# Performance work log

Measured on AMD Instinct MI355X. Metric: run time of the kernel, lower is better.

The kernel has to match this reference:

```python
import jax, jax.numpy as jnp
import numpy as np

EPS = 1e-6  # flax LayerNorm default

def layer_norm(x, scale, bias):
    mean = jnp.mean(x, axis=-1, keepdims=True)
    var = jnp.mean(jnp.square(x - mean), axis=-1, keepdims=True)
    return (x - mean) * jax.lax.rsqrt(var + EPS) * scale + bias

def setup_inputs() -> dict:
    key = jax.random.key(0)
    ks = jax.random.split(key, 8)
    B, M, D, R, H = 8, 8192, 512, 64, 128
    s = 0.02
    return {
        "memory": jax.random.normal(ks[0], (B, M, D), dtype=jnp.float32),
        "output_tokens": jax.random.normal(ks[1], (B, R, D), dtype=jnp.float32),
        # erase path params
        "ln_e_scale": jnp.ones((D,), jnp.float32),
        "ln_e_bias": jnp.zeros((D,), jnp.float32),
        "We1": jax.random.normal(ks[2], (D, H), dtype=jnp.float32) * s,
        "be1": jnp.zeros((H,), jnp.float32),
        "We2": jax.random.normal(ks[3], (H, R), dtype=jnp.float32) * s,
        "be2": jnp.zeros((R,), jnp.float32),
        # add path params
        "ln_a_scale": jnp.ones((D,), jnp.float32),
        "ln_a_bias": jnp.zeros((D,), jnp.float32),
        "Wa1": jax.random.normal(ks[4], (D, H), dtype=jnp.float32) * s,
        "ba1": jnp.zeros((H,), jnp.float32),
        "Wa2": jax.random.normal(ks[5], (H, D), dtype=jnp.float32) * s,
        "ba2": jnp.zeros((D,), jnp.float32),
    }

def reference(memory, output_tokens, ln_e_scale, ln_e_bias, We1, be1, We2, be2,
              ln_a_scale, ln_a_bias, Wa1, ba1, Wa2, ba2):
    # Erase weights: LN -> Dense(H) -> gelu -> Dense(r) -> transpose -> softmax over m
    e = layer_norm(memory, ln_e_scale, ln_e_bias)                  # [b,m,d]
    e = jax.nn.gelu(e @ We1 + be1)                                 # [b,m,H] (tanh approx, flax default)
    e = e @ We2 + be2                                              # [b,m,r]
    erase = jax.nn.softmax(jnp.transpose(e, (0, 2, 1)), axis=-1)   # [b,r,m], softmax over m
    # Add vectors: LN -> Dense(H) -> gelu -> Dense(d)
    a = layer_norm(output_tokens, ln_a_scale, ln_a_bias)           # [b,r,d]
    a = jax.nn.gelu(a @ Wa1 + ba1)                                 # [b,r,H]
    add = a @ Wa2 + ba2                                            # [b,r,d]
    # sum_r erase[b,r,m]*add[b,r,d] -> [b,m,d]; source builds a [b,r,m,d]
    # intermediate; this einsum is the identical math, fused as a batched matmul.
    ea = jnp.einsum('brm,brd->bmd', erase, add)
    # new_memory = memory * (1 - ea) + ea   (erase then add, add_matrix == ea)
    return memory * (1.0 - ea) + ea
```

## Files before the change

### kernel.cpp

```cpp
#include <hip/hip_runtime.h>
#include <hip/hip_bf16.h>
#include <math.h>

#define BB 8
#define MM 8192
#define DD 512
#define RR 64
#define HH 128

typedef __attribute__((ext_vector_type(8))) short bf16x8;
typedef __attribute__((ext_vector_type(4))) short bf16x4;
typedef __attribute__((ext_vector_type(4))) float f32x4;

#define XN_LD 520
#define H_LD  136

__device__ __forceinline__ float gelu_tanh(float x) {
    float u = 0.7978845608028654f * (x + 0.044715f * x * x * x);
    float e = __expf(2.0f * u);
    float t = 1.0f - 2.0f / (e + 1.0f);
    return 0.5f * x * (1.0f + t);
}

__device__ __forceinline__ short f2bf(float f) {
    unsigned int u = __float_as_uint(f);
    unsigned int r = u + 0x7FFFu + ((u >> 16) & 1u);
    return (short)(r >> 16);
}

__global__ __launch_bounds__(256) void prep_weights_kernel(
    const float* __restrict__ We1, const float* __restrict__ We2,
    short* __restrict__ We1T, short* __restrict__ We2T)
{
    int idx = blockIdx.x * 256 + threadIdx.x;
    if (idx < 128 * 512) {
        int n = idx >> 9, k = idx & 511;
        We1T[idx] = f2bf(We1[k * HH + n]);
    } else {
        int j = idx - 128 * 512;
        if (j < 64 * 128) {
            int n = j >> 7, k = j & 127;
            We2T[j] = f2bf(We2[k * RR + n]);
        }
    }
}

__global__ __launch_bounds__(256) void add_path_kernel(
    const float* __restrict__ ot, const float* __restrict__ scale,
    const float* __restrict__ bias, const float* __restrict__ Wa1,
    const float* __restrict__ ba1, const float* __restrict__ Wa2,
    const float* __restrict__ ba2, float* __restrict__ add_out)
{
    int tid = threadIdx.x;
    int b = blockIdx.x >> 6, r = blockIdx.x & 63;
    const float* x = ot + (size_t)(b * RR + r) * DD;
    __shared__ float xs[DD];
    __shared__ float hsm[HH];
    __shared__ float rs[4], rq[4];
    float v0 = x[tid], v1 = x[tid + 256];
    float s = v0 + v1, q = v0 * v0 + v1 * v1;
    #pragma unroll
    for (int off = 32; off > 0; off >>= 1) { s += __shfl_xor(s, off); q += __shfl_xor(q, off); }
    if ((tid & 63) == 0) { rs[tid >> 6] = s; rq[tid >> 6] = q; }
    __syncthreads();
    s = rs[0] + rs[1] + rs[2] + rs[3];
    q = rq[0] + rq[1] + rq[2] + rq[3];
    float mean = s * (1.0f / DD);
    float var = q * (1.0f / DD) - mean * mean;
    float inv = rsqrtf(var + 1e-6f);
    xs[tid]       = (v0 - mean) * inv * scale[tid]       + bias[tid];
    xs[tid + 256] = (v1 - mean) * inv * scale[tid + 256] + bias[tid + 256];
    __syncthreads();
    if (tid < HH) {
        float acc = ba1[tid];
        for (int k = 0; k < DD; k++) acc = fmaf(xs[k], Wa1[k * HH + tid], acc);
        hsm[tid] = gelu_tanh(acc);
    }
    __syncthreads();
    int d0 = tid, d1 = tid + 256;
    float a0 = ba2[d0], a1 = ba2[d1];
    #pragma unroll 4
    for (int k = 0; k < HH; k++) {
        float hk = hsm[k];
        a0 = fmaf(hk, Wa2[k * DD + d0], a0);
        a1 = fmaf(hk, Wa2[k * DD + d1], a1);
    }
    add_out[(size_t)(b * RR + r) * DD + d0] = a0;
    add_out[(size_t)(b * RR + r) * DD + d1] = a1;
}

__global__ __launch_bounds__(256) void erase_mfma_kernel(
    const float* __restrict__ mem, const float* __restrict__ scale,
    const float* __restrict__ bias, const short* __restrict__ We1T,
    const float* __restrict__ be1, const short* __restrict__ We2T,
    const float* __restrict__ be2, float* __restrict__ logits,
    float* __restrict__ pmax, float* __restrict__ psum)
{
    __shared__ short xn[32 * XN_LD];
    short* hsm = xn;

    int tid = threadIdx.x;
    int b = blockIdx.x >> 8;
    int chunk = blockIdx.x & 255;
    int m0 = chunk * 32;

    {
        int row = tid >> 3, sub = tid & 7;
        const float4* srcv = (const float4*)(mem + (size_t)(b * MM + m0 + row) * DD);
        float4 v[16];
        float s = 0.f, q = 0.f;
        #pragma unroll
        for (int j = 0; j < 16; j++) v[j] = srcv[j * 8 + sub];
        #pragma unroll
        for (int j = 0; j < 16; j++) {
            s += v[j].x + v[j].y + v[j].z + v[j].w;
            q += v[j].x*v[j].x + v[j].y*v[j].y + v[j].z*v[j].z + v[j].w*v[j].w;
        }
        #pragma unroll
        for (int off = 1; off <= 4; off <<= 1) { s += __shfl_xor(s, off); q += __shfl_xor(q, off); }
        float mean = s * (1.0f / 512.0f);
        float var = q * (1.0f / 512.0f) - mean * mean;
        float inv = rsqrtf(var + 1e-6f);
        const float4* scv = (const float4*)scale;
        const float4* biv = (const float4*)bias;
        #pragma unroll
        for (int j = 0; j < 16; j++) {
            float4 sc = scv[j * 8 + sub], bi = biv[j * 8 + sub];
            bf16x4 o;
            o[0] = f2bf((v[j].x - mean) * inv * sc.x + bi.x);
            o[1] = f2bf((v[j].y - mean) * inv * sc.y + bi.y);
            o[2] = f2bf((v[j].z - mean) * inv * sc.z + bi.z);
            o[3] = f2bf((v[j].w - mean) * inv * sc.w + bi.w);
            *(bf16x4*)&xn[row * XN_LD + j * 32 + sub * 4] = o;
        }
    }
    __syncthreads();

    int w = tid >> 6, l = tid & 63;
    int lr = l & 15, g = l >> 4, kg = g * 8;

    const short* bp0 = We1T + ((size_t)(w * 32 + lr) << 9) + kg;
    const short* bp1 = bp0 + (16 << 9);
    f32x4 acc00 = {0.f,0.f,0.f,0.f}, acc01 = acc00, acc10 = acc00, acc11 = acc00;
    #pragma unroll 4
    for (int ks = 0; ks < 16; ks++) {
        int k0 = ks * 32;
        bf16x8 a0 = *(const bf16x8*)&xn[lr * XN_LD + k0 + kg];
        bf16x8 a1 = *(const bf16x8*)&xn[(16 + lr) * XN_LD + k0 + kg];
        bf16x8 b0 = *(const bf16x8*)(bp0 + k0);
        bf16x8 b1 = *(const bf16x8*)(bp1 + k0);
        acc00 = __builtin_amdgcn_mfma_f32_16x16x32_bf16(a0, b0, acc00, 0, 0, 0);
        acc10 = __builtin_amdgcn_mfma_f32_16x16x32_bf16(a1, b0, acc10, 0, 0, 0);
        acc01 = __builtin_amdgcn_mfma_f32_16x16x32_bf16(a0, b1, acc01, 0, 0, 0);
        acc11 = __builtin_amdgcn_mfma_f32_16x16x32_bf16(a1, b1, acc11, 0, 0, 0);
    }
    __syncthreads();
    #pragma unroll
    for (int nf = 0; nf < 2; nf++) {
        int col = w * 32 + nf * 16 + lr;
        float bv = be1[col];
        f32x4 A0 = nf ? acc01 : acc00;
        f32x4 A1 = nf ? acc11 : acc10;
        #pragma unroll
        for (int rg = 0; rg < 4; rg++) {
            hsm[(g * 4 + rg) * H_LD + col]        = f2bf(gelu_tanh(A0[rg] + bv));
            hsm[(16 + g * 4 + rg) * H_LD + col]   = f2bf(gelu_tanh(A1[rg] + bv));
        }
    }
    __syncthreads();

    const short* bp2 = We2T + (w * 16 + lr) * 128 + kg;
    f32x4 c0 = {0.f,0.f,0.f,0.f}, c1 = c0;
    #pragma unroll
    for (int ks = 0; ks < 4; ks++) {
        int k0 = ks * 32;
        bf16x8 a0 = *(const bf16x8*)&hsm[lr * H_LD + k0 + kg];
        bf16x8 a1 = *(const bf16x8*)&hsm[(16 + lr) * H_LD + k0 + kg];
        bf16x8 bb = *(const bf16x8*)(bp2 + k0);
        c0 = __builtin_amdgcn_mfma_f32_16x16x32_bf16(a0, bb, c0, 0, 0, 0);
        c1 = __builtin_amdgcn_mfma_f32_16x16x32_bf16(a1, bb, c1, 0, 0, 0);
    }
    {
        int col = w * 16 + lr;
        float bv = be2[col];
        float vv[8];
        #pragma unroll
        for (int rg = 0; rg < 4; rg++) {
            vv[rg]     = c0[rg] + bv;
            vv[4 + rg] = c1[rg] + bv;
            logits[(size_t)(b * MM + m0 + g * 4 + rg) * 64 + col]      = vv[rg];
            logits[(size_t)(b * MM + m0 + 16 + g * 4 + rg) * 64 + col] = vv[4 + rg];
        }
        float mx = vv[0];
        #pragma unroll
        for (int j = 1; j < 8; j++) mx = fmaxf(mx, vv[j]);
        float sm = 0.f;
        #pragma unroll
        for (int j = 0; j < 8; j++) sm += __expf(vv[j] - mx);
        #pragma unroll
        for (int off = 16; off <= 32; off <<= 1) {
            float om = __shfl_xor(mx, off);
            float os = __shfl_xor(sm, off);
            float nm = fmaxf(mx, om);
            sm = sm * __expf(mx - nm) + os * __expf(om - nm);
            mx = nm;
        }
        if (l < 16) {
            pmax[((size_t)b * 256 + chunk) * 64 + col] = mx;
            psum[((size_t)b * 256 + chunk) * 64 + col] = sm;
        }
    }
}

__global__ __launch_bounds__(256) void softmax_finalize_kernel(
    const float* __restrict__ pmax, const float* __restrict__ psum,
    float* __restrict__ rmax, float* __restrict__ rinv)
{
    int b = blockIdx.x;
    int g = threadIdx.x >> 6, r = threadIdx.x & 63;
    float mx = -1e30f, sm = 0.0f;
    for (int ch = g; ch < 256; ch += 4) {
        float m2 = pmax[((size_t)b * 256 + ch) * 64 + r];
        float s2 = psum[((size_t)b * 256 + ch) * 64 + r];
        float nm = fmaxf(mx, m2);
        sm = sm * __expf(mx - nm) + s2 * __expf(m2 - nm);
        mx = nm;
    }
    __shared__ float sx_[4][64], sm_[4][64];
    sx_[g][r] = mx; sm_[g][r] = sm;
    __syncthreads();
    if (threadIdx.x < 64) {
        float M_ = sx_[0][threadIdx.x], S_ = sm_[0][threadIdx.x];
        #pragma unroll
        for (int gg = 1; gg < 4; gg++) {
            float m2 = sx_[gg][threadIdx.x], s2 = sm_[gg][threadIdx.x];
            float nm = fmaxf(M_, m2);
            S_ = S_ * __expf(M_ - nm) + s2 * __expf(m2 - nm);
            M_ = nm;
        }
        rmax[b * 64 + threadIdx.x] = M_;
        rinv[b * 64 + threadIdx.x] = 1.0f / S_;
    }
}

__global__ __launch_bounds__(256) void scale_transpose_kernel(
    const float* __restrict__ add, const float* __restrict__ rinv,
    short* __restrict__ addT)
{
    int b = blockIdx.x >> 3;
    int part = blockIdx.x & 7;
    const float* rv = rinv + b * 64;
    #pragma unroll
    for (int i = 0; i < 16; i++) {
        int idx = part * 4096 + threadIdx.x + i * 256;
        int d = idx >> 6, r = idx & 63;
        addT[(size_t)b * 32768 + idx] =
            f2bf(add[((size_t)b * 64 + r) * 512 + d] * rv[r]);
    }
}

__global__ __launch_bounds__(256, 4) void apply_mfma_kernel(
    const float* __restrict__ mem, const float* __restrict__ logits,
    const short* __restrict__ addT, const float* __restrict__ rmax,
    float* __restrict__ out)
{
    int tid = threadIdx.x;
    int w = tid >> 6, l = tid & 63;
    int b = blockIdx.x >> 7;
    int mt = blockIdx.x & 127;
    int m0 = mt * 64;
    int lr = l & 15, kg = (l >> 4) * 8;
    int nbase = w * 128;
    const short* aT = addT + (size_t)b * 512 * 64;

    float rm0[8], rm1[8];
    #pragma unroll
    for (int j = 0; j < 8; j++) {
        rm0[j] = rmax[b * 64 + kg + j];
        rm1[j] = rmax[b * 64 + 32 + kg + j];
    }

    for (int ms = 0; ms < 4; ms++) {
        float mv[8][4];
        #pragma unroll
        for (int nf = 0; nf < 8; nf++) {
            int d = nbase + nf * 16 + lr;
            #pragma unroll
            for (int rg = 0; rg < 4; rg++) {
                int m = m0 + ms * 16 + (l >> 4) * 4 + rg;
                mv[nf][rg] = mem[(size_t)(b * MM + m) * DD + d];
            }
        }
        int mrow = m0 + ms * 16 + lr;
        const float* lp = logits + (size_t)(b * MM + mrow) * 64 + kg;
        float w0[8], w1[8];
        #pragma unroll
        for (int j = 0; j < 8; j++) {
            w0[j] = __expf(lp[j]      - rm0[j]);
            w1[j] = __expf(lp[32 + j] - rm1[j]);
        }
        bf16x8 a0, a1;
        #pragma unroll
        for (int j = 0; j < 8; j++) { a0[j] = f2bf(w0[j]); a1[j] = f2bf(w1[j]); }

        f32x4 acc[8];
        #pragma unroll
        for (int nf = 0; nf < 8; nf++) {
            int d = nbase + nf * 16 + lr;
            bf16x8 b0 = *(const bf16x8*)&aT[d * 64 + kg];
            bf16x8 b1 = *(const bf16x8*)&aT[d * 64 + 32 + kg];
            f32x4 c = (f32x4){0.f, 0.f, 0.f, 0.f};
            c = __builtin_amdgcn_mfma_f32_16x16x32_bf16(a0, b0, c, 0, 0, 0);
            c = __builtin_amdgcn_mfma_f32_16x16x32_bf16(a1, b1, c, 0, 0, 0);
            acc[nf] = c;
        }
        #pragma unroll
        for (int nf = 0; nf < 8; nf++) {
            int d = nbase + nf * 16 + lr;
            #pragma unroll
            for (int rg = 0; rg < 4; rg++) {
                int m = m0 + ms * 16 + (l >> 4) * 4 + rg;
                size_t off = (size_t)(b * MM + m) * DD + d;
                float mvv = mv[nf][rg];
                out[off] = fmaf(acc[nf][rg], 1.0f - mvv, mvv);
            }
        }
    }
}

extern "C" void kernel_launch(void* const* d_in, const int* in_sizes, int n_in,
                              void* d_out, int out_size, void* d_ws, size_t ws_size,
                              hipStream_t stream) {
    const float* memory = (const float*)d_in[0];
    const float* ot     = (const float*)d_in[1];
    const float* ln_e_s = (const float*)d_in[2];
    const float* ln_e_b = (const float*)d_in[3];
    const float* We1    = (const float*)d_in[4];
    const float* be1    = (const float*)d_in[5];
    const float* We2    = (const float*)d_in[6];
    const float* be2    = (const float*)d_in[7];
    const float* ln_a_s = (const float*)d_in[8];
    const float* ln_a_b = (const float*)d_in[9];
    const float* Wa1    = (const float*)d_in[10];
    const float* ba1    = (const float*)d_in[11];
    const float* Wa2    = (const float*)d_in[12];
    const float* ba2    = (const float*)d_in[13];
    float* out = (float*)d_out;

    float* ws      = (float*)d_ws;
    float* add_ws  = ws;
    float* logits  = ws + 262144;
    float* pmaxw   = ws + 262144 + 4194304;
    float* psumw   = pmaxw + 131072;
    float* rmaxw   = psumw + 131072;
    float* rinvw   = rmaxw + 512;
    short* We1T    = (short*)(rinvw + 512);
    short* We2T    = We1T + 128 * 512;
    short* addT    = We2T + 64 * 128;

    hipLaunchKernelGGL(prep_weights_kernel, dim3(288), dim3(256), 0, stream,
                       We1, We2, We1T, We2T);
    hipLaunchKernelGGL(add_path_kernel, dim3(BB * RR), dim3(256), 0, stream,
                       ot, ln_a_s, ln_a_b, Wa1, ba1, Wa2, ba2, add_ws);
    hipLaunchKernelGGL(erase_mfma_kernel, dim3(BB * 256), dim3(256), 0, stream,
                       memory, ln_e_s, ln_e_b, We1T, be1, We2T, be2, logits, pmaxw, psumw);
    hipLaunchKernelGGL(softmax_finalize_kernel, dim3(BB), dim3(256), 0, stream,
                       pmaxw, psumw, rmaxw, rinvw);
    hipLaunchKernelGGL(scale_transpose_kernel, dim3(BB * 8), dim3(256), 0, stream,
                       add_ws, rinvw, addT);
    hipLaunchKernelGGL(apply_mfma_kernel, dim3(BB * 128), dim3(256), 0, stream,
                       memory, logits, addT, rmaxw, out);
}
```

Before: 195.5 us.

## Double erase-kernel threads and halve apply-kernel tile to raise parallelism

The erase kernel now runs 512 threads per block. Each wave computes one 16-column slice of the first GEMM, and in the second GEMM waves split across the two 16-row halves and the four column groups. Partial softmax stats are now emitted per half-chunk, so the finalize kernel reduces over 512 chunks. The apply kernel now uses 32-row tiles with twice as many blocks, giving more blocks to fill the GPU at the cost of less reuse of addT per block and more partial-stat traffic.

Measured after the change: 198.1 us. Within noise of the previous version (+1.3%).

```diff
diff --git a/kernel.cpp b/kernel.cpp
--- a/kernel.cpp
+++ b/kernel.cpp
@@ -89,7 +89,7 @@
     add_out[(size_t)(b * RR + r) * DD + d1] = a1;
 }
 
-__global__ __launch_bounds__(256) void erase_mfma_kernel(
+__global__ __launch_bounds__(512) void erase_mfma_kernel(
     const float* __restrict__ mem, const float* __restrict__ scale,
     const float* __restrict__ bias, const short* __restrict__ We1T,
     const float* __restrict__ be1, const short* __restrict__ We2T,
@@ -105,33 +105,33 @@
     int m0 = chunk * 32;
 
     {
-        int row = tid >> 3, sub = tid & 7;
+        int row = tid >> 4, sub = tid & 15;
         const float4* srcv = (const float4*)(mem + (size_t)(b * MM + m0 + row) * DD);
-        float4 v[16];
+        float4 v[8];
+        #pragma unroll
+        for (int j = 0; j < 8; j++) v[j] = srcv[j * 16 + sub];
         float s = 0.f, q = 0.f;
         #pragma unroll
-        for (int j = 0; j < 16; j++) v[j] = srcv[j * 8 + sub];
-        #pragma unroll
-        for (int j = 0; j < 16; j++) {
+        for (int j = 0; j < 8; j++) {
             s += v[j].x + v[j].y + v[j].z + v[j].w;
             q += v[j].x*v[j].x + v[j].y*v[j].y + v[j].z*v[j].z + v[j].w*v[j].w;
         }
         #pragma unroll
-        for (int off = 1; off <= 4; off <<= 1) { s += __shfl_xor(s, off); q += __shfl_xor(q, off); }
+        for (int off = 1; off <= 8; off <<= 1) { s += __shfl_xor(s, off); q += __shfl_xor(q, off); }
         float mean = s * (1.0f / 512.0f);
         float var = q * (1.0f / 512.0f) - mean * mean;
         float inv = rsqrtf(var + 1e-6f);
         const float4* scv = (const float4*)scale;
         const float4* biv = (const float4*)bias;
         #pragma unroll
-        for (int j = 0; j < 16; j++) {
-            float4 sc = scv[j * 8 + sub], bi = biv[j * 8 + sub];
+        for (int j = 0; j < 8; j++) {
+            float4 sc = scv[j * 16 + sub], bi = biv[j * 16 + sub];
             bf16x4 o;
             o[0] = f2bf((v[j].x - mean) * inv * sc.x + bi.x);
             o[1] = f2bf((v[j].y - mean) * inv * sc.y + bi.y);
             o[2] = f2bf((v[j].z - mean) * inv * sc.z + bi.z);
             o[3] = f2bf((v[j].w - mean) * inv * sc.w + bi.w);
-            *(bf16x4*)&xn[row * XN_LD + j * 32 + sub * 4] = o;
+            *(bf16x4*)&xn[row * XN_LD + (j * 16 + sub) * 4] = o;
         }
     }
     __syncthreads();
@@ -139,64 +139,50 @@
     int w = tid >> 6, l = tid & 63;
     int lr = l & 15, g = l >> 4, kg = g * 8;
 
-    const short* bp0 = We1T + ((size_t)(w * 32 + lr) << 9) + kg;
-    const short* bp1 = bp0 + (16 << 9);
-    f32x4 acc00 = {0.f,0.f,0.f,0.f}, acc01 = acc00, acc10 = acc00, acc11 = acc00;
+    const short* bp0 = We1T + ((size_t)(w * 16 + lr) << 9) + kg;
+    f32x4 acc0 = {0.f,0.f,0.f,0.f}, acc1 = acc0;
     #pragma unroll 4
     for (int ks = 0; ks < 16; ks++) {
         int k0 = ks * 32;
         bf16x8 a0 = *(const bf16x8*)&xn[lr * XN_LD + k0 + kg];
         bf16x8 a1 = *(const bf16x8*)&xn[(16 + lr) * XN_LD + k0 + kg];
         bf16x8 b0 = *(const bf16x8*)(bp0 + k0);
-        bf16x8 b1 = *(const bf16x8*)(bp1 + k0);
-        acc00 = __builtin_amdgcn_mfma_f32_16x16x32_bf16(a0, b0, acc00, 0, 0, 0);
-        acc10 = __builtin_amdgcn_mfma_f32_16x16x32_bf16(a1, b0, acc10, 0, 0, 0);
-        acc01 = __builtin_amdgcn_mfma_f32_16x16x32_bf16(a0, b1, acc01, 0, 0, 0);
-        acc11 = __builtin_amdgcn_mfma_f32_16x16x32_bf16(a1, b1, acc11, 0, 0, 0);
-    }
-    __syncthreads();
-    #pragma unroll
-    for (int nf = 0; nf < 2; nf++) {
-        int col = w * 32 + nf * 16 + lr;
+        acc0 = __builtin_amdgcn_mfma_f32_16x16x32_bf16(a0, b0, acc0, 0, 0, 0);
+        acc1 = __builtin_amdgcn_mfma_f32_16x16x32_bf16(a1, b0, acc1, 0, 0, 0);
+    }
+    __syncthreads();
+    {
+        int col = w * 16 + lr;
         float bv = be1[col];
-        f32x4 A0 = nf ? acc01 : acc00;
-        f32x4 A1 = nf ? acc11 : acc10;
         #pragma unroll
         for (int rg = 0; rg < 4; rg++) {
-            hsm[(g * 4 + rg) * H_LD + col]        = f2bf(gelu_tanh(A0[rg] + bv));
-            hsm[(16 + g * 4 + rg) * H_LD + col]   = f2bf(gelu_tanh(A1[rg] + bv));
-        }
-    }
-    __syncthreads();
-
-    const short* bp2 = We2T + (w * 16 + lr) * 128 + kg;
-    f32x4 c0 = {0.f,0.f,0.f,0.f}, c1 = c0;
+            hsm[(g * 4 + rg) * H_LD + col]      = f2bf(gelu_tanh(acc0[rg] + bv));
+            hsm[(16 + g * 4 + rg) * H_LD + col] = f2bf(gelu_tanh(acc1[rg] + bv));
+        }
+    }
+    __syncthreads();
+
+    int mhalf = w & 1, nf2 = w >> 1;
+    const short* bp2 = We2T + (nf2 * 16 + lr) * 128 + kg;
+    f32x4 c0 = {0.f,0.f,0.f,0.f};
     #pragma unroll
     for (int ks = 0; ks < 4; ks++) {
-        int k0 = ks * 32;
-        bf16x8 a0 = *(const bf16x8*)&hsm[lr * H_LD + k0 + kg];
-        bf16x8 a1 = *(const bf16x8*)&hsm[(16 + lr) * H_LD + k0 + kg];
-        bf16x8 bb = *(const bf16x8*)(bp2 + k0);
-        c0 = __builtin_amdgcn_mfma_f32_16x16x32_bf16(a0, bb, c0, 0, 0, 0);
-        c1 = __builtin_amdgcn_mfma_f32_16x16x32_bf16(a1, bb, c1, 0, 0, 0);
+        bf16x8 a2 = *(const bf16x8*)&hsm[(mhalf * 16 + lr) * H_LD + ks * 32 + kg];
+        bf16x8 bb = *(const bf16x8*)(bp2 + ks * 32);
+        c0 = __builtin_amdgcn_mfma_f32_16x16x32_bf16(a2, bb, c0, 0, 0, 0);
     }
     {
-        int col = w * 16 + lr;
-        float bv = be2[col];
-        float vv[8];
+        int c = nf2 * 16 + lr;
+        float bv = be2[c];
+        float vv[4];
         #pragma unroll
         for (int rg = 0; rg < 4; rg++) {
-            vv[rg]     = c0[rg] + bv;
-            vv[4 + rg] = c1[rg] + bv;
-            logits[(size_t)(b * MM + m0 + g * 4 + rg) * 64 + col]      = vv[rg];
-            logits[(size_t)(b * MM + m0 + 16 + g * 4 + rg) * 64 + col] = vv[4 + rg];
-        }
-        float mx = vv[0];
-        #pragma unroll
-        for (int j = 1; j < 8; j++) mx = fmaxf(mx, vv[j]);
-        float sm = 0.f;
-        #pragma unroll
-        for (int j = 0; j < 8; j++) sm += __expf(vv[j] - mx);
+            vv[rg] = c0[rg] + bv;
+            logits[(size_t)(b * MM + m0 + mhalf * 16 + g * 4 + rg) * 64 + c] = vv[rg];
+        }
+        float mx = fmaxf(fmaxf(vv[0], vv[1]), fmaxf(vv[2], vv[3]));
+        float sm = __expf(vv[0] - mx) + __expf(vv[1] - mx)
+                 + __expf(vv[2] - mx) + __expf(vv[3] - mx);
         #pragma unroll
         for (int off = 16; off <= 32; off <<= 1) {
             float om = __shfl_xor(mx, off);
@@ -206,8 +192,9 @@
             mx = nm;
         }
         if (l < 16) {
-            pmax[((size_t)b * 256 + chunk) * 64 + col] = mx;
-            psum[((size_t)b * 256 + chunk) * 64 + col] = sm;
+            int ch2 = chunk * 2 + mhalf;
+            pmax[((size_t)b * 512 + ch2) * 64 + c] = mx;
+            psum[((size_t)b * 512 + ch2) * 64 + c] = sm;
         }
     }
 }
@@ -219,9 +206,9 @@
     int b = blockIdx.x;
     int g = threadIdx.x >> 6, r = threadIdx.x & 63;
     float mx = -1e30f, sm = 0.0f;
-    for (int ch = g; ch < 256; ch += 4) {
-        float m2 = pmax[((size_t)b * 256 + ch) * 64 + r];
-        float s2 = psum[((size_t)b * 256 + ch) * 64 + r];
+    for (int ch = g; ch < 512; ch += 4) {
+        float m2 = pmax[((size_t)b * 512 + ch) * 64 + r];
+        float s2 = psum[((size_t)b * 512 + ch) * 64 + r];
         float nm = fmaxf(mx, m2);
         sm = sm * __expf(mx - nm) + s2 * __expf(m2 - nm);
         mx = nm;
@@ -266,9 +253,9 @@
 {
     int tid = threadIdx.x;
     int w = tid >> 6, l = tid & 63;
-    int b = blockIdx.x >> 7;
-    int mt = blockIdx.x & 127;
-    int m0 = mt * 64;
+    int b = blockIdx.x >> 8;
+    int mt = blockIdx.x & 255;
+    int m0 = mt * 32;
     int lr = l & 15, kg = (l >> 4) * 8;
     int nbase = w * 128;
     const short* aT = addT + (size_t)b * 512 * 64;
@@ -280,7 +267,7 @@
         rm1[j] = rmax[b * 64 + 32 + kg + j];
     }
 
-    for (int ms = 0; ms < 4; ms++) {
+    for (int ms = 0; ms < 2; ms++) {
         float mv[8][4];
         #pragma unroll
         for (int nf = 0; nf < 8; nf++) {
@@ -351,8 +338,8 @@
     float* add_ws  = ws;
     float* logits  = ws + 262144;
     float* pmaxw   = ws + 262144 + 4194304;
-    float* psumw   = pmaxw + 131072;
-    float* rmaxw   = psumw + 131072;
+    float* psumw   = pmaxw + 262144;
+    float* rmaxw   = psumw + 262144;
     float* rinvw   = rmaxw + 512;
     short* We1T    = (short*)(rinvw + 512);
     short* We2T    = We1T + 128 * 512;
@@ -362,12 +349,12 @@
                        We1, We2, We1T, We2T);
     hipLaunchKernelGGL(add_path_kernel, dim3(BB * RR), dim3(256), 0, stream,
                        ot, ln_a_s, ln_a_b, Wa1, ba1, Wa2, ba2, add_ws);
-    hipLaunchKernelGGL(erase_mfma_kernel, dim3(BB * 256), dim3(256), 0, stream,
+    hipLaunchKernelGGL(erase_mfma_kernel, dim3(BB * 256), dim3(512), 0, stream,
                        memory, ln_e_s, ln_e_b, We1T, be1, We2T, be2, logits, pmaxw, psumw);
     hipLaunchKernelGGL(softmax_finalize_kernel, dim3(BB), dim3(256), 0, stream,
                        pmaxw, psumw, rmaxw, rinvw);
     hipLaunchKernelGGL(scale_transpose_kernel, dim3(BB * 8), dim3(256), 0, stream,
                        add_ws, rinvw, addT);
-    hipLaunchKernelGGL(apply_mfma_kernel, dim3(BB * 128), dim3(256), 0, stream,
+    hipLaunchKernelGGL(apply_mfma_kernel, dim3(BB * 256), dim3(256), 0, stream,
                        memory, logits, addT, rmaxw, out);
 }
```
